# Optimization experiments

Measured on AMD Instinct MI355X. Metric: run time of the kernel, lower is better.

## Reference

```python
import jax, jax.numpy as jnp
import numpy as np

D_MODEL = 512
HEADS = 8
HEAD_DIM = D_MODEL // HEADS
TOPK = 16
BIAS_BASE = 1.0
SCALE = 1.0 / np.sqrt(HEAD_DIM)


def setup_inputs() -> dict:
    key = jax.random.key(0)
    ks = jax.random.split(key, 8)
    B, N, T, D = 8, 128, 64, D_MODEL
    h_val = jax.random.normal(ks[0], (B, N, T, D), dtype=jnp.float32)
    h_map = jax.random.normal(ks[1], (B, N, T, D), dtype=jnp.float32)
    base_adj = jax.random.uniform(ks[2], (B, N, N), dtype=jnp.float32)
    std = 0.02
    q_w = jax.random.normal(ks[3], (D, D), dtype=jnp.float32) * std
    k_w = jax.random.normal(ks[4], (D, D), dtype=jnp.float32) * std
    v_w = jax.random.normal(ks[5], (D, D), dtype=jnp.float32) * std
    o_w = jax.random.normal(ks[6], (D, D), dtype=jnp.float32) * std
    # residual_scale parameter: shape [1, N, 1, 1], init 0.5 (clamped to [0,1])
    residual_scale = jnp.full((1, N, 1, 1), 0.5, dtype=jnp.float32)
    return {"h_val": h_val, "h_map": h_map, "base_adj": base_adj,
            "q_w": q_w, "k_w": k_w, "v_w": v_w, "o_w": o_w,
            "residual_scale": residual_scale}


def _topk_mask_scores(scores):
    # scores: [b, h, i, j]; keep top-k per row along j, -inf elsewhere.
    n = scores.shape[-1]
    if TOPK <= 0 or TOPK >= n:
        return scores
    _, idx = jax.lax.top_k(scores, TOPK)              # [b,h,i,k]
    mask = jax.nn.one_hot(idx, n, dtype=jnp.bool_).any(axis=-2)  # [b,h,i,j]
    return jnp.where(mask, scores, -jnp.inf)


def reference(h_val, h_map, base_adj, q_w, k_w, v_w, o_w, residual_scale):
    B, N, T, D = h_val.shape
    # segment summary over tokens
    z_map = h_map.mean(axis=2)                        # [B, N, D]
    # projections (nn.Linear without bias: x @ W.T)
    q = (z_map @ q_w.T).reshape(B, N, HEADS, HEAD_DIM).transpose(0, 2, 1, 3)  # [B,H,N,hd]
    k = (z_map @ k_w.T).reshape(B, N, HEADS, HEAD_DIM).transpose(0, 2, 1, 3)
    scores = jnp.einsum('bhid,bhjd->bhij', q, k) * SCALE
    # log-bias injection from base adjacency
    bias = jnp.log(jnp.clip(base_adj, 1e-12, None))   # [B,N,N]
    scores = scores + BIAS_BASE * bias[:, None]
    raw_attn = jax.nn.softmax(scores, axis=-1)
    attn = jax.nn.softmax(_topk_mask_scores(scores), axis=-1)
    v = (h_val @ v_w.T).reshape(B, N, T, HEADS, HEAD_DIM).transpose(0, 3, 1, 2, 4)  # [B,H,N,T,hd]
    mixed = jnp.einsum('bhij,bhjtd->bhitd', attn, v)  # [B,H,N,T,hd]
    mixed = mixed.transpose(0, 2, 3, 1, 4).reshape(B, N, T, D)
    mixed = mixed @ o_w.T
    scale = jnp.clip(residual_scale, 0.0, 1.0)        # [1,N,1,1]
    out = h_val + mixed * scale                       # dropout is identity (p=0 / eval)
    return out, attn.mean(axis=1), raw_attn.mean(axis=1)
```

## Files before the change

kernel.cpp:

```cpp
#include <hip/hip_runtime.h>
#include <math.h>

#define B_  8
#define N_  128
#define T_  64
#define D_  512
#define H_  8
#define HD_ 64

typedef __attribute__((ext_vector_type(4))) float  f32x4;
typedef __attribute__((ext_vector_type(8))) __bf16 bf16x8;

__device__ __forceinline__ void async_copy16(const void* g, void* l) {
  __builtin_amdgcn_global_load_lds(
      (const __attribute__((address_space(1))) unsigned int*)g,
      (__attribute__((address_space(3))) unsigned int*)l, 16, 0, 0);
}

__global__ __launch_bounds__(256) void zmap_kernel(const float* __restrict__ hmap,
                                                   float* __restrict__ z) {
  const int bn = blockIdx.x;
  const float* src = hmap + (size_t)bn * (T_ * D_);
  int d = threadIdx.x;
#pragma unroll
  for (int rep = 0; rep < 2; rep++, d += 256) {
    float s = 0.f;
#pragma unroll 8
    for (int t = 0; t < T_; t++) s += src[t * D_ + d];
    z[(size_t)bn * D_ + d] = s * (1.f / T_);
  }
}

__global__ __launch_bounds__(256) void cvt_kernel(const float* __restrict__ s,
                                                  __bf16* __restrict__ d) {
  size_t i = ((size_t)blockIdx.x * 256 + threadIdx.x) << 3;
  f32x4 a = *(const f32x4*)&s[i];
  f32x4 b = *(const f32x4*)&s[i + 4];
  bf16x8 o;
  o[0] = (__bf16)a[0]; o[1] = (__bf16)a[1]; o[2] = (__bf16)a[2]; o[3] = (__bf16)a[3];
  o[4] = (__bf16)b[0]; o[5] = (__bf16)b[1]; o[6] = (__bf16)b[2]; o[7] = (__bf16)b[3];
  *(bf16x8*)&d[i] = o;
}

__global__ __launch_bounds__(256) void qk_gemm(const float* __restrict__ A,
    const float* __restrict__ W, float* __restrict__ Out) {
  __shared__ __bf16 As[64][72];
  __shared__ __bf16 Bs[64][72];
  const int tid  = threadIdx.x;
  const int n0   = blockIdx.x * 64;
  const int m0   = blockIdx.y * 64;
  const int lane = tid & 63, wv = tid >> 6;
  const int quad = lane >> 4, l15 = lane & 15;
  const int sr   = tid >> 2;
  f32x4 acc[4] = {};
  for (int kc = 0; kc < 512; kc += 64) {
#pragma unroll
    for (int i = 0; i < 4; i++) {
      int c = ((tid & 3) << 2) + (i << 4);
      f32x4 v = *(const f32x4*)&A[(size_t)(m0 + sr) * 512 + kc + c];
      As[sr][c + 0] = (__bf16)v[0]; As[sr][c + 1] = (__bf16)v[1];
      As[sr][c + 2] = (__bf16)v[2]; As[sr][c + 3] = (__bf16)v[3];
      f32x4 w = *(const f32x4*)&W[(size_t)(n0 + sr) * 512 + kc + c];
      Bs[sr][c + 0] = (__bf16)w[0]; Bs[sr][c + 1] = (__bf16)w[1];
      Bs[sr][c + 2] = (__bf16)w[2]; Bs[sr][c + 3] = (__bf16)w[3];
    }
    __syncthreads();
#pragma unroll
    for (int ks = 0; ks < 64; ks += 32) {
      bf16x8 a = *(const bf16x8*)&As[(wv << 4) + l15][ks + (quad << 3)];
#pragma unroll
      for (int ct = 0; ct < 4; ct++) {
        bf16x8 b = *(const bf16x8*)&Bs[(ct << 4) + l15][ks + (quad << 3)];
        acc[ct] = __builtin_amdgcn_mfma_f32_16x16x32_bf16(a, b, acc[ct], 0, 0, 0);
      }
    }
    __syncthreads();
  }
#pragma unroll
  for (int ct = 0; ct < 4; ct++)
#pragma unroll
    for (int r = 0; r < 4; r++) {
      const size_t m = (size_t)m0 + (wv << 4) + (quad << 2) + r;
      const size_t n = (size_t)n0 + (ct << 4) + l15;
      Out[m * 512 + n] = acc[ct][r];
    }
}

template<int MODE>
__global__ __launch_bounds__(256) void gemm128(const __bf16* __restrict__ A,
    const __bf16* __restrict__ Wb, void* __restrict__ Out,
    const float* __restrict__ hval, const float* __restrict__ rscale) {
  __align__(16) __shared__ __bf16 As[128 * 64];
  __align__(16) __shared__ __bf16 Bs[128 * 64];
  const int tid = threadIdx.x;
  const int lane = tid & 63, wv = tid >> 6;
  const int n0 = blockIdx.x << 7;
  const int m0 = blockIdx.y << 7;
  const int quad = lane >> 4, l15 = lane & 15;
  const int mq = (wv >> 1) << 6, nq = (wv & 1) << 6;
  f32x4 acc[4][4] = {};

  for (int kc = 0; kc < 512; kc += 64) {
#pragma unroll
    for (int it = 0; it < 4; it++) {
      const int gb = (wv << 8) + (it << 6);
      const int s  = gb + lane;
      const int m  = s >> 3, c = (s & 7) ^ (m & 7);
      async_copy16(A  + (size_t)(m0 + m) * 512 + kc + (c << 3), &As[gb << 3]);
      async_copy16(Wb + (size_t)(n0 + m) * 512 + kc + (c << 3), &Bs[gb << 3]);
    }
    __syncthreads();
#pragma unroll
    for (int k0 = 0; k0 < 64; k0 += 32) {
      const int cc = (k0 >> 3) + quad;
      bf16x8 af[4], bfr[4];
#pragma unroll
      for (int mt = 0; mt < 4; mt++) {
        int m = mq + (mt << 4) + l15;
        af[mt] = *(const bf16x8*)&As[((m << 3) + (cc ^ (m & 7))) << 3];
      }
#pragma unroll
      for (int nt = 0; nt < 4; nt++) {
        int n = nq + (nt << 4) + l15;
        bfr[nt] = *(const bf16x8*)&Bs[((n << 3) + (cc ^ (n & 7))) << 3];
      }
#pragma unroll
      for (int mt = 0; mt < 4; mt++)
#pragma unroll
        for (int nt = 0; nt < 4; nt++)
          acc[mt][nt] = __builtin_amdgcn_mfma_f32_16x16x32_bf16(af[mt], bfr[nt],
                                                                acc[mt][nt], 0, 0, 0);
    }
    __syncthreads();
  }

#pragma unroll
  for (int mt = 0; mt < 4; mt++)
#pragma unroll
    for (int nt = 0; nt < 4; nt++)
#pragma unroll
      for (int r = 0; r < 4; r++) {
        const size_t m = (size_t)m0 + mq + (mt << 4) + (quad << 2) + r;
        const size_t n = (size_t)n0 + nq + (nt << 4) + l15;
        float val = acc[mt][nt][r];
        if (MODE == 1) {
          size_t b = m >> 13, j = (m >> 6) & 127, tt = m & 63;
          size_t h = n >> 6, e = n & 63;
          ((__bf16*)Out)[(((b * 8 + h) * 128 + j) * 64 + tt) * 64 + e] = (__bf16)val;
        } else {
          int i = (int)((m >> 6) & 127);
          float sc = fminf(fmaxf(rscale[i], 0.f), 1.f);
          ((float*)Out)[m * 512 + n] = hval[m * 512 + n] + val * sc;
        }
      }
}

__global__ __launch_bounds__(256) void scores_kernel(
    const float* __restrict__ qb, const float* __restrict__ kb,
    const float* __restrict__ adj, __bf16* __restrict__ attnw,
    float* __restrict__ attn_mean, float* __restrict__ raw_mean) {
  __shared__ float  qs[4][64];
  __shared__ __bf16 ks_[128][66];
  const int ig = blockIdx.x, bh = blockIdx.y;
  const int b = bh >> 3, h = bh & 7;
  const int tid = threadIdx.x;
  {
    int r = tid >> 1, cb = (tid & 1) << 5;
    const float* ksrc = kb + ((size_t)(b * 128 + r)) * 512 + h * 64 + cb;
#pragma unroll
    for (int v = 0; v < 8; v++) {
      f32x4 kv = *(const f32x4*)&ksrc[v * 4];
      ks_[r][cb + v * 4 + 0] = (__bf16)kv[0];
      ks_[r][cb + v * 4 + 1] = (__bf16)kv[1];
      ks_[r][cb + v * 4 + 2] = (__bf16)kv[2];
      ks_[r][cb + v * 4 + 3] = (__bf16)kv[3];
    }
  }
  {
    int r = tid >> 6, ln = tid & 63;
    qs[r][ln] = qb[((size_t)(b * 128 + (ig << 2) + r)) * 512 + h * 64 + ln];
  }
  __syncthreads();
  const int wv = tid >> 6, lane = tid & 63;
  const int i = (ig << 2) + wv;
  const int j0 = lane, j1 = lane + 64;
  float s0 = 0.f, s1 = 0.f;
#pragma unroll 16
  for (int e = 0; e < 64; e++) {
    float qe = qs[wv][e];
    s0 += qe * (float)ks_[j0][e];
    s1 += qe * (float)ks_[j1][e];
  }
  const size_t arow = ((size_t)b * 128 + i) * 128;
  s0 = s0 * 0.125f + logf(fmaxf(adj[arow + j0], 1e-12f));
  s1 = s1 * 0.125f + logf(fmaxf(adj[arow + j1], 1e-12f));
  float mx = fmaxf(s0, s1);
#pragma unroll
  for (int off = 32; off; off >>= 1) mx = fmaxf(mx, __shfl_xor(mx, off));
  float e0 = expf(s0 - mx), e1 = expf(s1 - mx);
  float sum = e0 + e1;
#pragma unroll
  for (int off = 32; off; off >>= 1) sum += __shfl_xor(sum, off);
  float inv = 0.125f / sum;
  atomicAdd(&raw_mean[arow + j0], e0 * inv);
  atomicAdd(&raw_mean[arow + j1], e1 * inv);
  float w0 = s0, w1 = s1;
  bool sel0 = false, sel1 = false;
  float m16 = 0.f, denom = 0.f;
  for (int it = 0; it < 16; it++) {
    float v; int idx;
    if (w1 > w0) { v = w1; idx = j1; } else { v = w0; idx = j0; }
#pragma unroll
    for (int off = 32; off; off >>= 1) {
      float ov = __shfl_xor(v, off);
      int   oi = __shfl_xor(idx, off);
      if (ov > v || (ov == v && oi < idx)) { v = ov; idx = oi; }
    }
    if (it == 0) m16 = v;
    denom += expf(v - m16);
    if (idx == j0) { sel0 = true; w0 = -INFINITY; }
    if (idx == j1) { sel1 = true; w1 = -INFINITY; }
  }
  const float invd = 1.f / denom;
  const float p0 = sel0 ? expf(s0 - m16) * invd : 0.f;
  const float p1 = sel1 ? expf(s1 - m16) * invd : 0.f;
  const size_t ab = ((size_t)bh * 128 + i) * 128;
  attnw[ab + j0] = (__bf16)p0;
  attnw[ab + j1] = (__bf16)p1;
  if (sel0) atomicAdd(&attn_mean[arow + j0], p0 * 0.125f);
  if (sel1) atomicAdd(&attn_mean[arow + j1], p1 * 0.125f);
}

__global__ __launch_bounds__(256) void mix_kernel(
    const __bf16* __restrict__ attnw, const __bf16* __restrict__ vbuf,
    __bf16* __restrict__ mixed) {
  __shared__ __bf16 As[128][136];
  __shared__ __bf16 Bt[64][136];
  const int nt = blockIdx.x;
  const int bh = blockIdx.y;
  const int b = bh >> 3, h = bh & 7;
  const int n0 = nt << 6;
  const int tid = threadIdx.x;
  {
    int i = tid >> 1, cb = (tid & 1) << 6;
    const __bf16* src = attnw + ((size_t)bh * 128 + i) * 128 + cb;
#pragma unroll
    for (int v = 0; v < 8; v++)
      *(bf16x8*)&As[i][cb + (v << 3)] = *(const bf16x8*)&src[v << 3];
  }
  {
    int j = tid >> 1, cb = (tid & 1) << 5;
    const __bf16* src = vbuf + ((size_t)bh * 128 + j) * 4096 + n0 + cb;
#pragma unroll
    for (int v = 0; v < 4; v++) {
      bf16x8 x = *(const bf16x8*)&src[v << 3];
#pragma unroll
      for (int u = 0; u < 8; u++) Bt[cb + (v << 3) + u][j] = x[u];
    }
  }
  __syncthreads();
  const int lane = tid & 63, wv = tid >> 6;
  const int quad = lane >> 4, l15 = lane & 15;
  f32x4 acc[2][4] = {};
#pragma unroll
  for (int kk = 0; kk < 128; kk += 32) {
    bf16x8 a0 = *(const bf16x8*)&As[(wv << 5) + l15][kk + (quad << 3)];
    bf16x8 a1 = *(const bf16x8*)&As[(wv << 5) + 16 + l15][kk + (quad << 3)];
#pragma unroll
    for (int ct = 0; ct < 4; ct++) {
      bf16x8 bb = *(const bf16x8*)&Bt[(ct << 4) + l15][kk + (quad << 3)];
      acc[0][ct] = __builtin_amdgcn_mfma_f32_16x16x32_bf16(a0, bb, acc[0][ct], 0, 0, 0);
      acc[1][ct] = __builtin_amdgcn_mfma_f32_16x16x32_bf16(a1, bb, acc[1][ct], 0, 0, 0);
    }
  }
  const int tt = nt;
#pragma unroll
  for (int rt = 0; rt < 2; rt++)
#pragma unroll
    for (int ct = 0; ct < 4; ct++)
#pragma unroll
      for (int r = 0; r < 4; r++) {
        int i = (wv << 5) + (rt << 4) + (quad << 2) + r;
        int e = (ct << 4) + l15;
        mixed[(((size_t)b * 128 + i) * 64 + tt) * 512 + h * 64 + e] =
            (__bf16)acc[rt][ct][r];
      }
}

extern "C" void kernel_launch(void* const* d_in, const int* in_sizes, int n_in,
                              void* d_out, int out_size, void* d_ws, size_t ws_size,
                              hipStream_t stream) {
  (void)in_sizes; (void)n_in; (void)out_size; (void)ws_size;
  const float* h_val = (const float*)d_in[0];
  const float* h_map = (const float*)d_in[1];
  const float* adj   = (const float*)d_in[2];
  const float* q_w   = (const float*)d_in[3];
  const float* k_w   = (const float*)d_in[4];
  const float* v_w   = (const float*)d_in[5];
  const float* o_w   = (const float*)d_in[6];
  const float* rsc   = (const float*)d_in[7];

  char* ws = (char*)d_ws;
  float*  zmap  = (float*)(ws);
  __bf16* vwb   = (__bf16*)(ws);
  __bf16* owb   = (__bf16*)(ws + (512ull << 10));
  float*  qb    = (float*)(ws + (2ull << 20));
  float*  kb    = (float*)(ws + (4ull << 20));
  __bf16* attnw = (__bf16*)(ws + (6ull << 20));
  __bf16* hvalb = (__bf16*)(ws + (8ull << 20));
  __bf16* mixed = (__bf16*)(ws + (8ull << 20));
  __bf16* vbuf  = (__bf16*)(ws + (72ull << 20));

  float* out       = (float*)d_out;
  float* attn_mean = out + 33554432ull;
  float* raw_mean  = attn_mean + 131072ull;

  zmap_kernel<<<1024, 256, 0, stream>>>(h_map, zmap);
  qk_gemm<<<dim3(8, 16), 256, 0, stream>>>(zmap, q_w, qb);
  qk_gemm<<<dim3(8, 16), 256, 0, stream>>>(zmap, k_w, kb);
  cvt_kernel<<<128, 256, 0, stream>>>(v_w, vwb);
  cvt_kernel<<<128, 256, 0, stream>>>(o_w, owb);
  cvt_kernel<<<16384, 256, 0, stream>>>(h_val, hvalb);
  hipMemsetAsync(attn_mean, 0, 2ull * 131072ull * sizeof(float), stream);
  scores_kernel<<<dim3(32, 64), 256, 0, stream>>>(qb, kb, adj, attnw, attn_mean, raw_mean);
  gemm128<1><<<dim3(4, 512), 256, 0, stream>>>(hvalb, vwb, vbuf, nullptr, nullptr);
  mix_kernel<<<dim3(64, 64), 256, 0, stream>>>(attnw, vbuf, mixed);
  gemm128<2><<<dim3(4, 512), 256, 0, stream>>>(mixed, owb, d_out, h_val, rsc);
}
```

Measured before the change: 545.0 us.

## Fuse h_val bf16 conversion into V-projection GEMM and vectorize zmap reduction

Removes the separate h_val fp32-to-bf16 conversion kernel and its 64MB bf16 round trip by loading fp32 tiles directly in the V-projection GEMM and converting them in registers before the swizzled LDS store. The zmap mean is rewritten to use float4 loads, with the token range split across two thread halves and combined through LDS. The residual scale is hoisted to a single per-block load. In exchange, the A-tile load in MODE 1 becomes synchronous register loads instead of async global-to-LDS copies. Since each h_val element is read by the four column blocks, the GEMM now reads fp32 data four times.

```diff
diff --git a/kernel.cpp b/kernel.cpp
--- a/kernel.cpp
+++ b/kernel.cpp
@@ -19,15 +19,23 @@
 
 __global__ __launch_bounds__(256) void zmap_kernel(const float* __restrict__ hmap,
                                                    float* __restrict__ z) {
+  __shared__ f32x4 red[128];
   const int bn = blockIdx.x;
-  const float* src = hmap + (size_t)bn * (T_ * D_);
-  int d = threadIdx.x;
-#pragma unroll
-  for (int rep = 0; rep < 2; rep++, d += 256) {
-    float s = 0.f;
+  const int c4 = threadIdx.x & 127;
+  const int th = threadIdx.x >> 7;
+  const float* src = hmap + (size_t)bn * (T_ * D_) + (size_t)th * 32 * D_ + c4 * 4;
+  f32x4 s = {0.f, 0.f, 0.f, 0.f};
 #pragma unroll 8
-    for (int t = 0; t < T_; t++) s += src[t * D_ + d];
-    z[(size_t)bn * D_ + d] = s * (1.f / T_);
+  for (int t = 0; t < 32; t++) {
+    f32x4 v = *(const f32x4*)&src[(size_t)t * D_];
+    s = s + v;
+  }
+  if (th) red[c4] = s;
+  __syncthreads();
+  if (!th) {
+    f32x4 r = red[c4];
+    f32x4 o = (s + r) * (1.f / 64.f);
+    *(f32x4*)&z[(size_t)bn * D_ + c4 * 4] = o;
   }
 }
 
@@ -88,8 +96,9 @@
 
 template<int MODE>
 __global__ __launch_bounds__(256) void gemm128(const __bf16* __restrict__ A,
-    const __bf16* __restrict__ Wb, void* __restrict__ Out,
-    const float* __restrict__ hval, const float* __restrict__ rscale) {
+    const float* __restrict__ Af, const __bf16* __restrict__ Wb,
+    void* __restrict__ Out, const float* __restrict__ hval,
+    const float* __restrict__ rscale) {
   __align__(16) __shared__ __bf16 As[128 * 64];
   __align__(16) __shared__ __bf16 Bs[128 * 64];
   const int tid = threadIdx.x;
@@ -100,14 +109,41 @@
   const int mq = (wv >> 1) << 6, nq = (wv & 1) << 6;
   f32x4 acc[4][4] = {};
 
+  float sc = 0.f;
+  if (MODE == 2) sc = fminf(fmaxf(rscale[((m0 + mq) >> 6) & 127], 0.f), 1.f);
+
   for (int kc = 0; kc < 512; kc += 64) {
-#pragma unroll
-    for (int it = 0; it < 4; it++) {
-      const int gb = (wv << 8) + (it << 6);
-      const int s  = gb + lane;
-      const int m  = s >> 3, c = (s & 7) ^ (m & 7);
-      async_copy16(A  + (size_t)(m0 + m) * 512 + kc + (c << 3), &As[gb << 3]);
-      async_copy16(Wb + (size_t)(n0 + m) * 512 + kc + (c << 3), &Bs[gb << 3]);
+    if (MODE == 1) {
+#pragma unroll
+      for (int it = 0; it < 4; it++) {
+        const int gb = (wv << 8) + (it << 6);
+        const int s  = gb + lane;
+        const int m  = s >> 3, c = (s & 7) ^ (m & 7);
+        async_copy16(Wb + (size_t)(n0 + m) * 512 + kc + (c << 3), &Bs[gb << 3]);
+      }
+#pragma unroll
+      for (int it = 0; it < 4; it++) {
+        const int s  = (wv << 8) + (it << 6) + lane;
+        const int m  = s >> 3, cp = s & 7;
+        const float* src = Af + (size_t)(m0 + m) * 512 + kc + (cp << 3);
+        f32x4 u0 = *(const f32x4*)src;
+        f32x4 u1 = *(const f32x4*)(src + 4);
+        bf16x8 o;
+        o[0] = (__bf16)u0[0]; o[1] = (__bf16)u0[1];
+        o[2] = (__bf16)u0[2]; o[3] = (__bf16)u0[3];
+        o[4] = (__bf16)u1[0]; o[5] = (__bf16)u1[1];
+        o[6] = (__bf16)u1[2]; o[7] = (__bf16)u1[3];
+        *(bf16x8*)&As[((m << 3) + (cp ^ (m & 7))) << 3] = o;
+      }
+    } else {
+#pragma unroll
+      for (int it = 0; it < 4; it++) {
+        const int gb = (wv << 8) + (it << 6);
+        const int s  = gb + lane;
+        const int m  = s >> 3, c = (s & 7) ^ (m & 7);
+        async_copy16(A  + (size_t)(m0 + m) * 512 + kc + (c << 3), &As[gb << 3]);
+        async_copy16(Wb + (size_t)(n0 + m) * 512 + kc + (c << 3), &Bs[gb << 3]);
+      }
     }
     __syncthreads();
 #pragma unroll
@@ -148,8 +184,6 @@
           size_t h = n >> 6, e = n & 63;
           ((__bf16*)Out)[(((b * 8 + h) * 128 + j) * 64 + tt) * 64 + e] = (__bf16)val;
         } else {
-          int i = (int)((m >> 6) & 127);
-          float sc = fminf(fmaxf(rscale[i], 0.f), 1.f);
           ((float*)Out)[m * 512 + n] = hval[m * 512 + n] + val * sc;
         }
       }
@@ -307,7 +341,6 @@
   float*  qb    = (float*)(ws + (2ull << 20));
   float*  kb    = (float*)(ws + (4ull << 20));
   __bf16* attnw = (__bf16*)(ws + (6ull << 20));
-  __bf16* hvalb = (__bf16*)(ws + (8ull << 20));
   __bf16* mixed = (__bf16*)(ws + (8ull << 20));
   __bf16* vbuf  = (__bf16*)(ws + (72ull << 20));
 
@@ -320,10 +353,9 @@
   qk_gemm<<<dim3(8, 16), 256, 0, stream>>>(zmap, k_w, kb);
   cvt_kernel<<<128, 256, 0, stream>>>(v_w, vwb);
   cvt_kernel<<<128, 256, 0, stream>>>(o_w, owb);
-  cvt_kernel<<<16384, 256, 0, stream>>>(h_val, hvalb);
   hipMemsetAsync(attn_mean, 0, 2ull * 131072ull * sizeof(float), stream);
   scores_kernel<<<dim3(32, 64), 256, 0, stream>>>(qb, kb, adj, attnw, attn_mean, raw_mean);
-  gemm128<1><<<dim3(4, 512), 256, 0, stream>>>(hvalb, vwb, vbuf, nullptr, nullptr);
+  gemm128<1><<<dim3(4, 512), 256, 0, stream>>>(nullptr, h_val, vwb, vbuf, nullptr, nullptr);
   mix_kernel<<<dim3(64, 64), 256, 0, stream>>>(attnw, vbuf, mixed);
-  gemm128<2><<<dim3(4, 512), 256, 0, stream>>>(mixed, owb, d_out, h_val, rsc);
-}
+  gemm128<2><<<dim3(4, 512), 256, 0, stream>>>(mixed, nullptr, owb, d_out, h_val, rsc);
+}
```

After: 539.0 us. About the same (-1.1%).
